# Kernel tuning notes

Measured on AMD Instinct MI355X. Metric: run time of the kernel, lower is better.

Reference implementation:

```python
import jax, jax.numpy as jnp
import numpy as np

NC, TOP_K, ALPHA, BETA, EPS = 80, 13, 1.0, 6.0, 1e-9
IMG = 640


def _make_anchors():
    pts = []
    for stride in (8, 16, 32):
        n = IMG // stride
        c = (np.arange(n, dtype=np.float32) + 0.5) * stride
        yy, xx = np.meshgrid(c, c, indexing='ij')
        pts.append(np.stack([xx.ravel(), yy.ravel()], axis=-1))
    return jnp.asarray(np.concatenate(pts, axis=0))  # (8400, 2)


def setup_inputs() -> dict:
    key = jax.random.key(0)
    ks = jax.random.split(key, 8)
    b, n_max = 32, 32
    anchor_points = _make_anchors()
    A = anchor_points.shape[0]
    pred_scores = jax.random.uniform(ks[0], (b, A, NC), dtype=jnp.float32)
    # predicted boxes: centers near anchors, sizes in [8, 72]
    ctr = anchor_points[None] + 5.0 * jax.random.normal(ks[1], (b, A, 2), dtype=jnp.float32)
    wh = 8.0 + 64.0 * jax.random.uniform(ks[2], (b, A, 2), dtype=jnp.float32)
    pred_bboxes = jnp.concatenate([ctr - wh / 2, ctr + wh / 2], axis=-1)
    # gt boxes: random centers in image, sizes in [20, 180]
    gctr = IMG * jax.random.uniform(ks[3], (b, n_max, 2), dtype=jnp.float32)
    gwh = 20.0 + 160.0 * jax.random.uniform(ks[4], (b, n_max, 2), dtype=jnp.float32)
    gt_bboxes = jnp.concatenate([gctr - gwh / 2, gctr + gwh / 2], axis=-1)
    gt_labels = jax.random.randint(ks[5], (b, n_max, 1), 0, NC, dtype=jnp.int64)
    n_valid = jax.random.randint(ks[6], (b,), 1, n_max + 1)
    mask_gt = (jnp.arange(n_max)[None, :] < n_valid[:, None]).astype(jnp.float32)[..., None]
    return {
        'pred_scores': pred_scores, 'pred_bboxes': pred_bboxes,
        'anchor_points': anchor_points, 'gt_labels': gt_labels,
        'gt_bboxes': gt_bboxes, 'mask_gt': mask_gt,
    }


def _iou_pairwise(gt, pd, eps=1e-7):
    # gt: (b,n,1,4), pd: (b,1,A,4) -> (b,n,A) elementwise-broadcast IoU
    lt = jnp.maximum(gt[..., :2], pd[..., :2])
    rb = jnp.minimum(gt[..., 2:], pd[..., 2:])
    inter = jnp.clip(rb - lt, 0).prod(-1)
    area_g = (gt[..., 2:] - gt[..., :2]).prod(-1)
    area_p = (pd[..., 2:] - pd[..., :2]).prod(-1)
    return inter / (area_g + area_p - inter + eps)


def reference(pred_scores, pred_bboxes, anchor_points, gt_labels, gt_bboxes, mask_gt):
    b, A, nc = pred_scores.shape
    n = gt_bboxes.shape[1]
    dt = pred_scores.dtype
    mg = mask_gt[..., 0] > 0  # (b,n) valid-gt mask

    # --- candidates whose anchor center lies inside the gt box ---
    lt, rb = gt_bboxes[:, :, None, :2], gt_bboxes[:, :, None, 2:]
    deltas = jnp.concatenate([anchor_points[None, None] - lt, rb - anchor_points[None, None]], axis=-1)
    mask_in_gts = deltas.min(-1) > EPS  # (b,n,A)
    valid = mask_in_gts & mg[:, :, None]

    # --- box metrics: class score gathered at gt label, IoU(gt, pred) ---
    lbl = jnp.clip(gt_labels[..., 0], 0, nc - 1)  # (b,n)
    ps = jnp.swapaxes(pred_scores, 1, 2)  # (b,nc,A)
    bbox_scores = jnp.take_along_axis(ps, lbl[:, :, None], axis=1)  # (b,n,A)
    bbox_scores = jnp.where(valid, bbox_scores, jnp.zeros((), dt))
    overlaps = jnp.clip(_iou_pairwise(gt_bboxes[:, :, None], pred_bboxes[:, None]), 0)
    overlaps = jnp.where(valid, overlaps, jnp.zeros((), dt))
    align_metric = bbox_scores ** ALPHA * overlaps ** BETA  # (b,n,A)

    # --- top-k candidate selection (duplicate indices zeroed, as in torch) ---
    _, idx = jax.lax.top_k(align_metric, TOP_K)  # (b,n,K)
    idx = jnp.where(mg[:, :, None], idx, 0)
    rows = jnp.arange(b * n)[:, None]
    counts = jnp.zeros((b * n, A), jnp.int32).at[rows, idx.reshape(b * n, TOP_K)].add(1)
    counts = counts.reshape(b, n, A)
    mask_topk = jnp.where(counts > 1, 0, counts).astype(dt)
    mask_pos = mask_topk * valid.astype(dt)  # (b,n,A)

    # --- resolve anchors assigned to multiple gts: keep highest IoU ---
    fg = mask_pos.sum(1)  # (b,A)
    is_max = jnp.swapaxes(jax.nn.one_hot(overlaps.argmax(1), n, dtype=dt), 1, 2)  # (b,n,A)
    mask_pos = jnp.where(fg[:, None, :] > 1, is_max, mask_pos)
    fg = mask_pos.sum(1)

    # --- gather targets ---
    tgi = mask_pos.argmax(1)  # (b,A)
    t_labels = jnp.take_along_axis(lbl, tgi, axis=1)  # (b,A), already >= 0
    target_bboxes = jnp.take_along_axis(gt_bboxes, tgi[:, :, None], axis=1)  # (b,A,4)
    target_scores = jax.nn.one_hot(t_labels, nc, dtype=dt)
    target_scores = jnp.where(fg[:, :, None] > 0, target_scores, jnp.zeros((), dt))

    # --- normalize scores by alignment metric ---
    am = align_metric * mask_pos
    pos_align = am.max(-1, keepdims=True)  # (b,n,1)
    pos_ov = (overlaps * mask_pos).max(-1, keepdims=True)
    norm = (am * pos_ov / (pos_align + EPS)).max(1)[:, :, None]  # (b,A,1)
    target_scores = target_scores * norm
    return target_bboxes, target_scores, fg > 0
```

## Files before the change

### kernel.cpp

```cpp
#include <hip/hip_runtime.h>

#define B_CNT 32
#define N_CNT 32
#define A_CNT 8400
#define NC_CNT 80
#define TOPK 13
#define EPS_IN 1e-9f

typedef unsigned long long u64;
typedef unsigned int u32;


__global__ void __launch_bounds__(256) k1(const float* __restrict__ ps, const float* __restrict__ pb,
        const float* __restrict__ ap, const int* __restrict__ gl,
        const float* __restrict__ gb, const float* __restrict__ mgt,
        int* __restrict__ cIdx, float* __restrict__ cAl, float* __restrict__ cOv) {
    __shared__ u64 wmax[TOPK][4];
    __shared__ u64 winsh[TOPK];
    int bn = blockIdx.x;
    int b = bn >> 5;
    float4 g = ((const float4*)gb)[bn];
    bool mg = mgt[bn] > 0.f;
    int lbl = min(max(gl[bn], 0), NC_CNT - 1);
    float area_g = (g.z - g.x) * (g.w - g.y);
    const float*  psb = ps + (size_t)b * A_CNT * NC_CNT;
    const float4* pbb = (const float4*)(pb + (size_t)b * A_CNT * 4);
    const float2* ap2 = (const float2*)ap;
    int tid = threadIdx.x;

    u64 keys[TOPK];
#pragma unroll
    for (int j = 0; j < TOPK; j++) keys[j] = 0;

    for (int a = tid; a < A_CNT; a += 256) {
        float2 aq = ap2[a];
        float dmin = fminf(fminf(aq.x - g.x, aq.y - g.y), fminf(g.z - aq.x, g.w - aq.y));
        bool v = mg && (dmin > EPS_IN);
        float al = 0.f;
        if (v) {
            float4 p = pbb[a];
            float ix = fminf(g.z, p.z) - fmaxf(g.x, p.x);
            float iy = fminf(g.w, p.w) - fmaxf(g.y, p.y);
            float inter = fmaxf(ix, 0.f) * fmaxf(iy, 0.f);
            float area_p = (p.z - p.x) * (p.w - p.y);
            float ov = inter / (area_g + area_p - inter + 1e-7f);
            ov = fmaxf(ov, 0.f);
            float sc = psb[(size_t)a * NC_CNT + lbl];
            float o2 = ov * ov;
            al = sc * (o2 * o2 * o2);
        }
        u64 kc = ((u64)__float_as_uint(al) << 32) | (u64)(0xFFFFFFFFu - (u32)a);
        if (kc > keys[TOPK - 1]) {
            keys[TOPK - 1] = kc;
#pragma unroll
            for (int j = TOPK - 1; j > 0; --j) {
                if (keys[j] > keys[j - 1]) { u64 t2 = keys[j]; keys[j] = keys[j - 1]; keys[j - 1] = t2; }
            }
        }
    }

    int wid = tid >> 6;
    for (int pass = 0; pass < TOPK; ++pass) {
        u64 m = keys[0];
#pragma unroll
        for (int off = 1; off <= 32; off <<= 1) {
            u64 o = __shfl_xor(m, off);
            if (o > m) m = o;
        }
        if ((tid & 63) == 0) wmax[pass][wid] = m;
        __syncthreads();
        u64 w = wmax[pass][0];
#pragma unroll
        for (int q = 1; q < 4; q++) { u64 o = wmax[pass][q]; if (o > w) w = o; }
        if (tid == 0) winsh[pass] = w;
        bool f = false;
#pragma unroll
        for (int j = 0; j < TOPK - 1; ++j) {
            f = f || (keys[j] == w);
            keys[j] = f ? keys[j + 1] : keys[j];
        }
        f = f || (keys[TOPK - 1] == w);
        if (f) keys[TOPK - 1] = 0;
    }
    __syncthreads();

    if (tid < TOPK) {
        u64 w = winsh[tid];
        int i = (int)(0xFFFFFFFFu - (u32)(w & 0xFFFFFFFFull));
        float al = __uint_as_float((u32)(w >> 32));
        float2 aq = ap2[i];
        float dmin = fminf(fminf(aq.x - g.x, aq.y - g.y), fminf(g.z - aq.x, g.w - aq.y));
        bool v = mg && (dmin > EPS_IN);
        int ci = -1; float ov = 0.f;
        if (v) {
            float4 p = pbb[i];
            float ix = fminf(g.z, p.z) - fmaxf(g.x, p.x);
            float iy = fminf(g.w, p.w) - fmaxf(g.y, p.y);
            float inter = fmaxf(ix, 0.f) * fmaxf(iy, 0.f);
            float area_p = (p.z - p.x) * (p.w - p.y);
            ov = inter / (area_g + area_p - inter + 1e-7f);
            ov = fmaxf(ov, 0.f);
            ci = i;
        }
        cIdx[bn * TOPK + tid] = ci;
        cAl [bn * TOPK + tid] = v ? al : 0.f;
        cOv [bn * TOPK + tid] = ov;
    }
}

__global__ void __launch_bounds__(256) k2(const float* __restrict__ ps, const float* __restrict__ pb,
        const float* __restrict__ ap, const int* __restrict__ gl,
        const float* __restrict__ gb, const float* __restrict__ mgt,
        const int* __restrict__ cIdx, const float* __restrict__ cAl, const float* __restrict__ cOv,
        int* __restrict__ tgi, float* __restrict__ alT, float* __restrict__ fgw,
        int* __restrict__ posAl, int* __restrict__ posOv) {
    __shared__ int   sIdx[N_CNT][TOPK];
    __shared__ float sAl[N_CNT][TOPK];
    __shared__ float sOv[N_CNT][TOPK];
    __shared__ float4 gs[N_CNT];
    __shared__ float  mgs[N_CNT];
    __shared__ int    lbls[N_CNT];
    int b = blockIdx.y;
    if (threadIdx.x < N_CNT) {
        int bn = b * N_CNT + threadIdx.x;
        gs[threadIdx.x]   = ((const float4*)gb)[bn];
        mgs[threadIdx.x]  = mgt[bn];
        lbls[threadIdx.x] = min(max(gl[bn], 0), NC_CNT - 1);
    }
    for (int t = threadIdx.x; t < N_CNT * TOPK; t += 256) {
        int r = t / TOPK, k = t - r * TOPK;
        int src = b * N_CNT * TOPK + t;
        sIdx[r][k] = cIdx[src];
        sAl [r][k] = cAl [src];
        sOv [r][k] = cOv [src];
    }
    __syncthreads();
    int a = blockIdx.x * 256 + threadIdx.x;
    if (a >= A_CNT) return;
    size_t ba = (size_t)b * A_CNT + a;

    int fg = 0, t = 0, mk = -1;
    for (int nn = 0; nn < N_CNT; nn++) {
        int m = -1;
#pragma unroll
        for (int k = 0; k < TOPK; k++)
            if (sIdx[nn][k] == a) m = k;
        if (m >= 0) { if (fg == 0) { t = nn; mk = m; } fg++; }
    }

    float al = 0.f, fgv = 0.f;
    if (fg == 1) {
        al = sAl[t][mk];
        float ov = sOv[t][mk];
        atomicMax(&posAl[b * N_CNT + t], __float_as_int(al));
        atomicMax(&posOv[b * N_CNT + t], __float_as_int(ov));
        fgv = 1.f;
    } else if (fg > 1) {
        float ax = ap[2 * a], ay = ap[2 * a + 1];
        float4 p = ((const float4*)pb)[ba];
        float area_p = (p.z - p.x) * (p.w - p.y);
        float bo = -1.f; int bt = 0;
        for (int nn = 0; nn < N_CNT; nn++) {
            float4 g = gs[nn];
            float dmin = fminf(fminf(ax - g.x, ay - g.y), fminf(g.z - ax, g.w - ay));
            bool v = (mgs[nn] > 0.f) && (dmin > EPS_IN);
            float ov = 0.f;
            if (v) {
                float ix = fminf(g.z, p.z) - fmaxf(g.x, p.x);
                float iy = fminf(g.w, p.w) - fmaxf(g.y, p.y);
                float inter = fmaxf(ix, 0.f) * fmaxf(iy, 0.f);
                float area_g = (g.z - g.x) * (g.w - g.y);
                ov = inter / (area_g + area_p - inter + 1e-7f);
                ov = fmaxf(ov, 0.f);
            }
            if (ov > bo) { bo = ov; bt = nn; }
        }
        t = bt;
        float sc = ps[ba * NC_CNT + lbls[t]];
        float o2 = bo * bo;
        al = sc * (o2 * o2 * o2);
        atomicMax(&posAl[b * N_CNT + t], __float_as_int(al));
        atomicMax(&posOv[b * N_CNT + t], __float_as_int(bo));
        fgv = 1.f;
    }
    tgi[ba] = t;
    alT[ba] = al;
    fgw[ba] = fgv;
}

__global__ void __launch_bounds__(256) k3(const int* __restrict__ tgi, const float* __restrict__ alT,
        const float* __restrict__ fgw, const int* __restrict__ posAl, const int* __restrict__ posOv,
        const int* __restrict__ gl, const float* __restrict__ gb,
        float* __restrict__ out_bbox, float* __restrict__ out_scores, float* __restrict__ out_fg) {
    int idx = blockIdx.x * 256 + threadIdx.x;
    if (idx >= B_CNT * A_CNT * (NC_CNT / 4)) return;
    int ba = idx / 20;
    int q  = idx - ba * 20;
    int b  = ba / A_CNT;
    int t  = tgi[ba];
    int bn = b * N_CNT + t;
    float fgv = fgw[ba];
    float norm = 0.f;
    if (fgv > 0.f) {
        float pa = __int_as_float(posAl[bn]);
        float po = __int_as_float(posOv[bn]);
        norm = alT[ba] * po / (pa + 1e-9f);
    }
    int lbl = min(max(gl[bn], 0), NC_CNT - 1);
    int c0 = q * 4;
    float4 v;
    v.x = (fgv > 0.f && lbl == c0    ) ? norm : 0.f;
    v.y = (fgv > 0.f && lbl == c0 + 1) ? norm : 0.f;
    v.z = (fgv > 0.f && lbl == c0 + 2) ? norm : 0.f;
    v.w = (fgv > 0.f && lbl == c0 + 3) ? norm : 0.f;
    ((float4*)out_scores)[idx] = v;
    if (q == 0) {
        ((float4*)out_bbox)[ba] = ((const float4*)gb)[bn];
        out_fg[ba] = fgv;
    }
}

extern "C" void kernel_launch(void* const* d_in, const int* in_sizes, int n_in,
                              void* d_out, int out_size, void* d_ws, size_t ws_size,
                              hipStream_t stream) {
    const float* pred_scores   = (const float*)d_in[0];
    const float* pred_bboxes   = (const float*)d_in[1];
    const float* anchor_points = (const float*)d_in[2];
    const int*   gt_labels     = (const int*)d_in[3];
    const float* gt_bboxes     = (const float*)d_in[4];
    const float* mask_gt       = (const float*)d_in[5];

    const int BA = B_CNT * A_CNT;
    const int BN = B_CNT * N_CNT;

    char* w = (char*)d_ws;
    int*   posAl   = (int*)w;                  w += (size_t)BN * 4;
    int*   posOv   = (int*)w;                  w += (size_t)BN * 4;
    int*   cIdx    = (int*)w;                  w += (size_t)BN * TOPK * 4;
    float* cAl     = (float*)w;                w += (size_t)BN * TOPK * 4;
    float* cOv     = (float*)w;                w += (size_t)BN * TOPK * 4;
    int*   tgi     = (int*)w;                  w += (size_t)BA * 4;
    float* alT     = (float*)w;                w += (size_t)BA * 4;
    float* fgw     = (float*)w;                w += (size_t)BA * 4;

    float* out_bbox   = (float*)d_out;
    float* out_scores = out_bbox + (size_t)BA * 4;
    float* out_fg     = out_scores + (size_t)BA * NC_CNT;

    hipMemsetAsync(posAl, 0, (size_t)2 * BN * 4, stream);

    dim3 blk(256);
    k1<<<dim3(BN), blk, 0, stream>>>(pred_scores, pred_bboxes, anchor_points,
                                     gt_labels, gt_bboxes, mask_gt,
                                     cIdx, cAl, cOv);
    k2<<<dim3((A_CNT + 255) / 256, B_CNT), blk, 0, stream>>>(pred_scores, pred_bboxes,
                                     anchor_points, gt_labels, gt_bboxes, mask_gt,
                                     cIdx, cAl, cOv,
                                     tgi, alT, fgw, posAl, posOv);
    k3<<<dim3((BA * (NC_CNT / 4) + 255) / 256), blk, 0, stream>>>(tgi, alT, fgw,
                                     posAl, posOv, gt_labels, gt_bboxes,
                                     out_bbox, out_scores, out_fg);
}
```

Measured before the change: 212.1 us.

## Scatter top-k candidates sparsely in assignment kernel and widen top-k blocks

The per-anchor assignment kernel, which scanned all 32×13 candidates for every anchor, is replaced by a per-batch kernel. One thread per candidate builds a bitmask of the gts that selected the same anchor, and only the first owner writes that anchor's result and performs the atomics. Untouched anchors now get their zero defaults from a larger memset of the workspace. The top-k kernel moves to 1024-thread blocks, so each thread keeps a shorter 9-entry local list, with a wider cross-wave reduction. This trades a dense per-anchor scan for sparse work, at the cost of extra memset traffic and only 32 blocks in the assignment kernel.

```diff
diff --git a/kernel.cpp b/kernel.cpp
--- a/kernel.cpp
+++ b/kernel.cpp
@@ -5,17 +5,19 @@
 #define A_CNT 8400
 #define NC_CNT 80
 #define TOPK 13
+#define KCAP 9
 #define EPS_IN 1e-9f
 
 typedef unsigned long long u64;
 typedef unsigned int u32;
 
 
-__global__ void __launch_bounds__(256) k1(const float* __restrict__ ps, const float* __restrict__ pb,
-        const float* __restrict__ ap, const int* __restrict__ gl,
-        const float* __restrict__ gb, const float* __restrict__ mgt,
+__global__ void __launch_bounds__(1024, 8) k1(const float* __restrict__ ps,
+        const float* __restrict__ pb, const float* __restrict__ ap,
+        const int* __restrict__ gl, const float* __restrict__ gb,
+        const float* __restrict__ mgt,
         int* __restrict__ cIdx, float* __restrict__ cAl, float* __restrict__ cOv) {
-    __shared__ u64 wmax[TOPK][4];
+    __shared__ u64 wmax[TOPK][16];
     __shared__ u64 winsh[TOPK];
     int bn = blockIdx.x;
     int b = bn >> 5;
@@ -28,11 +30,11 @@
     const float2* ap2 = (const float2*)ap;
     int tid = threadIdx.x;
 
-    u64 keys[TOPK];
-#pragma unroll
-    for (int j = 0; j < TOPK; j++) keys[j] = 0;
-
-    for (int a = tid; a < A_CNT; a += 256) {
+    u64 keys[KCAP];
+#pragma unroll
+    for (int j = 0; j < KCAP; j++) keys[j] = 0;
+
+    for (int a = tid; a < A_CNT; a += 1024) {
         float2 aq = ap2[a];
         float dmin = fminf(fminf(aq.x - g.x, aq.y - g.y), fminf(g.z - aq.x, g.w - aq.y));
         bool v = mg && (dmin > EPS_IN);
@@ -50,10 +52,10 @@
             al = sc * (o2 * o2 * o2);
         }
         u64 kc = ((u64)__float_as_uint(al) << 32) | (u64)(0xFFFFFFFFu - (u32)a);
-        if (kc > keys[TOPK - 1]) {
-            keys[TOPK - 1] = kc;
-#pragma unroll
-            for (int j = TOPK - 1; j > 0; --j) {
+        if (kc > keys[KCAP - 1]) {
+            keys[KCAP - 1] = kc;
+#pragma unroll
+            for (int j = KCAP - 1; j > 0; --j) {
                 if (keys[j] > keys[j - 1]) { u64 t2 = keys[j]; keys[j] = keys[j - 1]; keys[j - 1] = t2; }
             }
         }
@@ -71,16 +73,16 @@
         __syncthreads();
         u64 w = wmax[pass][0];
 #pragma unroll
-        for (int q = 1; q < 4; q++) { u64 o = wmax[pass][q]; if (o > w) w = o; }
+        for (int q = 1; q < 16; q++) { u64 o = wmax[pass][q]; if (o > w) w = o; }
         if (tid == 0) winsh[pass] = w;
         bool f = false;
 #pragma unroll
-        for (int j = 0; j < TOPK - 1; ++j) {
+        for (int j = 0; j < KCAP - 1; ++j) {
             f = f || (keys[j] == w);
             keys[j] = f ? keys[j + 1] : keys[j];
         }
-        f = f || (keys[TOPK - 1] == w);
-        if (f) keys[TOPK - 1] = 0;
+        f = f || (keys[KCAP - 1] == w);
+        if (f) keys[KCAP - 1] = 0;
     }
     __syncthreads();
 
@@ -108,9 +110,10 @@
     }
 }
 
-__global__ void __launch_bounds__(256) k2(const float* __restrict__ ps, const float* __restrict__ pb,
-        const float* __restrict__ ap, const int* __restrict__ gl,
-        const float* __restrict__ gb, const float* __restrict__ mgt,
+__global__ void __launch_bounds__(448) k2(const float* __restrict__ ps,
+        const float* __restrict__ pb, const float* __restrict__ ap,
+        const int* __restrict__ gl, const float* __restrict__ gb,
+        const float* __restrict__ mgt,
         const int* __restrict__ cIdx, const float* __restrict__ cAl, const float* __restrict__ cOv,
         int* __restrict__ tgi, float* __restrict__ alT, float* __restrict__ fgw,
         int* __restrict__ posAl, int* __restrict__ posOv) {
@@ -120,14 +123,15 @@
     __shared__ float4 gs[N_CNT];
     __shared__ float  mgs[N_CNT];
     __shared__ int    lbls[N_CNT];
-    int b = blockIdx.y;
-    if (threadIdx.x < N_CNT) {
-        int bn = b * N_CNT + threadIdx.x;
-        gs[threadIdx.x]   = ((const float4*)gb)[bn];
-        mgs[threadIdx.x]  = mgt[bn];
-        lbls[threadIdx.x] = min(max(gl[bn], 0), NC_CNT - 1);
-    }
-    for (int t = threadIdx.x; t < N_CNT * TOPK; t += 256) {
+    int b = blockIdx.x;
+    int tid = threadIdx.x;
+    if (tid < N_CNT) {
+        int bn = b * N_CNT + tid;
+        gs[tid]   = ((const float4*)gb)[bn];
+        mgs[tid]  = mgt[bn];
+        lbls[tid] = min(max(gl[bn], 0), NC_CNT - 1);
+    }
+    for (int t = tid; t < N_CNT * TOPK; t += 448) {
         int r = t / TOPK, k = t - r * TOPK;
         int src = b * N_CNT * TOPK + t;
         sIdx[r][k] = cIdx[src];
@@ -135,34 +139,34 @@
         sOv [r][k] = cOv [src];
     }
     __syncthreads();
-    int a = blockIdx.x * 256 + threadIdx.x;
-    if (a >= A_CNT) return;
-    size_t ba = (size_t)b * A_CNT + a;
-
-    int fg = 0, t = 0, mk = -1;
+    if (tid >= N_CNT * TOPK) return;
+    int n = tid / TOPK, k = tid - n * TOPK;
+    int i = sIdx[n][k];
+    if (i < 0) return;
+
+    unsigned int m = 0;
     for (int nn = 0; nn < N_CNT; nn++) {
-        int m = -1;
-#pragma unroll
-        for (int k = 0; k < TOPK; k++)
-            if (sIdx[nn][k] == a) m = k;
-        if (m >= 0) { if (fg == 0) { t = nn; mk = m; } fg++; }
-    }
-
-    float al = 0.f, fgv = 0.f;
+        bool has = false;
+#pragma unroll
+        for (int kk = 0; kk < TOPK; kk++) has = has || (sIdx[nn][kk] == i);
+        m |= (has ? 1u : 0u) << nn;
+    }
+    int fg = __popc(m);
+    int first = __ffs(m) - 1;
+    if (n != first) return;
+
+    size_t ba = (size_t)b * A_CNT + i;
+    int t, lw; float al, ovw;
     if (fg == 1) {
-        al = sAl[t][mk];
-        float ov = sOv[t][mk];
-        atomicMax(&posAl[b * N_CNT + t], __float_as_int(al));
-        atomicMax(&posOv[b * N_CNT + t], __float_as_int(ov));
-        fgv = 1.f;
-    } else if (fg > 1) {
-        float ax = ap[2 * a], ay = ap[2 * a + 1];
+        t = n; al = sAl[n][k]; ovw = sOv[n][k];
+    } else {
+        float2 aq = ((const float2*)ap)[i];
         float4 p = ((const float4*)pb)[ba];
         float area_p = (p.z - p.x) * (p.w - p.y);
         float bo = -1.f; int bt = 0;
         for (int nn = 0; nn < N_CNT; nn++) {
             float4 g = gs[nn];
-            float dmin = fminf(fminf(ax - g.x, ay - g.y), fminf(g.z - ax, g.w - ay));
+            float dmin = fminf(fminf(aq.x - g.x, aq.y - g.y), fminf(g.z - aq.x, g.w - aq.y));
             bool v = (mgs[nn] > 0.f) && (dmin > EPS_IN);
             float ov = 0.f;
             if (v) {
@@ -179,13 +183,14 @@
         float sc = ps[ba * NC_CNT + lbls[t]];
         float o2 = bo * bo;
         al = sc * (o2 * o2 * o2);
-        atomicMax(&posAl[b * N_CNT + t], __float_as_int(al));
-        atomicMax(&posOv[b * N_CNT + t], __float_as_int(bo));
-        fgv = 1.f;
-    }
+        ovw = bo;
+    }
+    lw = b * N_CNT + t;
     tgi[ba] = t;
     alT[ba] = al;
-    fgw[ba] = fgv;
+    fgw[ba] = 1.f;
+    atomicMax(&posAl[lw], __float_as_int(al));
+    atomicMax(&posOv[lw], __float_as_int(ovw));
 }
 
 __global__ void __launch_bounds__(256) k3(const int* __restrict__ tgi, const float* __restrict__ alT,
@@ -236,28 +241,27 @@
     char* w = (char*)d_ws;
     int*   posAl   = (int*)w;                  w += (size_t)BN * 4;
     int*   posOv   = (int*)w;                  w += (size_t)BN * 4;
+    int*   tgi     = (int*)w;                  w += (size_t)BA * 4;
+    float* alT     = (float*)w;                w += (size_t)BA * 4;
+    float* fgw     = (float*)w;                w += (size_t)BA * 4;
     int*   cIdx    = (int*)w;                  w += (size_t)BN * TOPK * 4;
     float* cAl     = (float*)w;                w += (size_t)BN * TOPK * 4;
     float* cOv     = (float*)w;                w += (size_t)BN * TOPK * 4;
-    int*   tgi     = (int*)w;                  w += (size_t)BA * 4;
-    float* alT     = (float*)w;                w += (size_t)BA * 4;
-    float* fgw     = (float*)w;                w += (size_t)BA * 4;
 
     float* out_bbox   = (float*)d_out;
     float* out_scores = out_bbox + (size_t)BA * 4;
     float* out_fg     = out_scores + (size_t)BA * NC_CNT;
 
-    hipMemsetAsync(posAl, 0, (size_t)2 * BN * 4, stream);
-
-    dim3 blk(256);
-    k1<<<dim3(BN), blk, 0, stream>>>(pred_scores, pred_bboxes, anchor_points,
-                                     gt_labels, gt_bboxes, mask_gt,
-                                     cIdx, cAl, cOv);
-    k2<<<dim3((A_CNT + 255) / 256, B_CNT), blk, 0, stream>>>(pred_scores, pred_bboxes,
-                                     anchor_points, gt_labels, gt_bboxes, mask_gt,
-                                     cIdx, cAl, cOv,
-                                     tgi, alT, fgw, posAl, posOv);
-    k3<<<dim3((BA * (NC_CNT / 4) + 255) / 256), blk, 0, stream>>>(tgi, alT, fgw,
-                                     posAl, posOv, gt_labels, gt_bboxes,
-                                     out_bbox, out_scores, out_fg);
-}
+    hipMemsetAsync(posAl, 0, ((size_t)2 * BN + (size_t)3 * BA) * 4, stream);
+
+    k1<<<dim3(BN), dim3(1024), 0, stream>>>(pred_scores, pred_bboxes, anchor_points,
+                                            gt_labels, gt_bboxes, mask_gt,
+                                            cIdx, cAl, cOv);
+    k2<<<dim3(B_CNT), dim3(448), 0, stream>>>(pred_scores, pred_bboxes, anchor_points,
+                                              gt_labels, gt_bboxes, mask_gt,
+                                              cIdx, cAl, cOv,
+                                              tgi, alT, fgw, posAl, posOv);
+    k3<<<dim3((BA * (NC_CNT / 4) + 255) / 256), dim3(256), 0, stream>>>(tgi, alT, fgw,
+                                              posAl, posOv, gt_labels, gt_bboxes,
+                                              out_bbox, out_scores, out_fg);
+}
```

Result: slower. 256.7 us (+21.1%).
